# Kernel optimization log

Measured on AMD Instinct MI355X. Metric: run time of the kernel, lower is better.

Reference implementation:

```python
import jax, jax.numpy as jnp
import numpy as np

NUM_NODES = 100000
EMBED_DIM = 128
COMP_DIM = 64
T = 8
NSUB = 50000


def layer_norm(x, g, b, eps=1e-5):
    mu = jnp.mean(x, axis=-1, keepdims=True)
    var = jnp.mean((x - mu) ** 2, axis=-1, keepdims=True)
    return (x - mu) * jax.lax.rsqrt(var + eps) * g + b


def setup_inputs() -> dict:
    key = jax.random.key(0)
    ks = jax.random.split(key, 12)
    D, C = EMBED_DIM, COMP_DIM
    s = lambda n: 1.0 / np.sqrt(n)
    return {
        "x": jax.random.normal(ks[0], (T * NSUB, D), dtype=jnp.float32),
        "indices": jax.random.randint(ks[1], (T, NSUB), 0, NUM_NODES, dtype=jnp.int64),
        "bd": jax.random.normal(ks[2], (NUM_NODES, D), dtype=jnp.float32),
        "ln_d_g": jnp.ones((D,), jnp.float32), "ln_d_b": jnp.zeros((D,), jnp.float32),
        "Wd1": jax.random.normal(ks[3], (D, 2 * D), jnp.float32) * s(D),
        "bd1": jnp.zeros((2 * D,), jnp.float32),
        "Wd2": jax.random.normal(ks[4], (2 * D, C), jnp.float32) * s(2 * D),
        "bd2": jnp.zeros((C,), jnp.float32),
        "ln_u_g": jnp.ones((C,), jnp.float32), "ln_u_b": jnp.zeros((C,), jnp.float32),
        "Wu1": jax.random.normal(ks[5], (C, 2 * C), jnp.float32) * s(C),
        "bu1": jnp.zeros((2 * C,), jnp.float32),
        "Wu2": jax.random.normal(ks[6], (2 * C, D), jnp.float32) * s(2 * C),
        "bu2": jnp.zeros((D,), jnp.float32),
    }


def reference(x, indices, bd, ln_d_g, ln_d_b, Wd1, bd1, Wd2, bd2,
              ln_u_g, ln_u_b, Wu1, bu1, Wu2, bu2):
    # _to_entire: per-timestep scatter-add of subnode feats into full node table
    x3 = x.reshape(T, NSUB, EMBED_DIM)  # [T, Nsub, D]
    scattered = jax.vmap(
        lambda xt, it: jax.ops.segment_sum(xt, it, num_segments=NUM_NODES)
    )(x3, indices)  # [T, num_nodes, D]
    inp = scattered + bd[None]  # ta + bd (use_bd=True)
    h = layer_norm(inp, ln_d_g, ln_d_b)
    # mlp_d: Linear -> GELU -> Dropout(eval=identity) -> Linear
    h = jax.nn.gelu(h @ Wd1 + bd1, approximate=False) @ Wd2 + bd2  # [T, num_nodes, C]
    # _from_entire: gather activated rows per timestep, then LN + mlp_u
    gathered = jax.vmap(lambda ht, it: ht[it])(h, indices)  # [T, Nsub, C]
    g = gathered.reshape(T * NSUB, COMP_DIM)
    u = layer_norm(g, ln_u_g, ln_u_b)
    out = jax.nn.gelu(u @ Wu1 + bu1, approximate=False) @ Wu2 + bu2  # [T*Nsub, D]
    return out
```

## Files before the change

### kernel.cpp

```cpp
#include <hip/hip_runtime.h>
#include <math.h>

#define NN 100000
#define DD 128
#define CC 64
#define TT 8
#define NS 50000
#define G8 8
#define MAXS 391
#define MAXS_B 196
#define T1MAX (G8 * MAXS)
#define T2MAX (G8 * MAXS_B)
#define L2CAP 25000
#define ZINT4 200032

typedef __attribute__((ext_vector_type(4))) float f32x4;
typedef __attribute__((ext_vector_type(8))) short bf16x8;
typedef unsigned short ushort_t;

__device__ __forceinline__ short f2bf(float f) {
    union { float f; unsigned u; } v; v.f = f;
    unsigned r = v.u + 0x7fffu + ((v.u >> 16) & 1u);
    return (short)(r >> 16);
}
__device__ __forceinline__ unsigned pk_bf16(float lo, float hi) {
    unsigned r;
    asm("v_cvt_pk_bf16_f32 %0, %1, %2" : "=v"(r) : "v"(lo), "v"(hi));
    return r;
}
__device__ __forceinline__ float gelu(float x) {
    float t = x + 0.044715f * x * x * x;
    return x / (1.0f + __expf(-1.5957691216f * t));
}

__global__ void prep_all(const float* __restrict__ Wd1, const float* __restrict__ Wd2,
                         const float* __restrict__ Wu1, const float* __restrict__ Wu2,
                         short* __restrict__ pW1, short* __restrict__ pW2,
                         short* __restrict__ pW3, short* __restrict__ pW4,
                         int4* __restrict__ zbase) {
    int b = blockIdx.x;
    if (b >= 36) {
        int i = (b - 36) * 256 + threadIdx.x;
        if (i < ZINT4) zbase[i] = (int4){0, 0, 0, 0};
// ... 57 lines not shown
}

__device__ __forceinline__ void ln_d_pack(
    const float (&v)[32], int kgrp,
    const float* __restrict__ lndg, const float* __restrict__ lndb, bf16x8 (&afr)[4]) {
    float s1 = 0.f;
    #pragma unroll
    for (int j = 0; j < 32; ++j) s1 += v[j];
    s1 += __shfl_xor(s1, 16); s1 += __shfl_xor(s1, 32);
    float mu = s1 * 0.0078125f;
    float s2 = 0.f;
    #pragma unroll
    for (int j = 0; j < 32; ++j) { float d = v[j] - mu; s2 += d * d; }
    s2 += __shfl_xor(s2, 16); s2 += __shfl_xor(s2, 32);
    float rs = rsqrtf(s2 * 0.0078125f + 1e-5f);
    union U8 { bf16x8 v8; unsigned u[4]; };
    const float* gp = lndg + kgrp * 8;
    const float* bbp = lndb + kgrp * 8;
    #pragma unroll
    for (int ks = 0; ks < 4; ++ks) {
        float4 g0 = *(const float4*)(gp + ks * 32);
        float4 g1 = *(const float4*)(gp + ks * 32 + 4);
        float4 c0 = *(const float4*)(bbp + ks * 32);
        float4 c1 = *(const float4*)(bbp + ks * 32 + 4);
        U8 t;
        t.u[0] = pk_bf16((v[ks*8+0]-mu)*rs*g0.x + c0.x, (v[ks*8+1]-mu)*rs*g0.y + c0.y);
        t.u[1] = pk_bf16((v[ks*8+2]-mu)*rs*g0.z + c0.z, (v[ks*8+3]-mu)*rs*g0.w + c0.w);
        t.u[2] = pk_bf16((v[ks*8+4]-mu)*rs*g1.x + c1.x, (v[ks*8+5]-mu)*rs*g1.y + c1.y);
        t.u[3] = pk_bf16((v[ks*8+6]-mu)*rs*g1.z + c1.z, (v[ks*8+7]-mu)*rs*g1.w + c1.w);
        afr[ks] = t.v8;
    }
}

__device__ __forceinline__ void mlp_core(
    const bf16x8 (&afr)[4], short* myb, int arow, int kgrp,
    const short* sW1, const short* sW2, const short* __restrict__ pW3, const short* sW4,
    const float* __restrict__ bd1, const float* __restrict__ bd2,
    const float* __restrict__ lnug, const float* __restrict__ lnub,
    const float* __restrict__ bu1, f32x4 (&acc4)[8]) {
    const int lane = kgrp * 16 + arow;
    f32x4 acc2[4];
    #pragma unroll
    for (int n = 0; n < 4; ++n) acc2[n] = (f32x4){0.f, 0.f, 0.f, 0.f};
    for (int ks2 = 0; ks2 < 8; ++ks2) {
        f32x4 a1v[2];
        a1v[0] = (f32x4){0.f, 0.f, 0.f, 0.f};
        a1v[1] = (f32x4){0.f, 0.f, 0.f, 0.f};
        #pragma unroll
        for (int ks1 = 0; ks1 < 4; ++ks1) {
            #pragma unroll
            for (int p = 0; p < 2; ++p) {
                bf16x8 bf = *(const bf16x8*)(sW1 + (size_t)((((2 * ks2 + p) << 2) | ks1) * 64 + lane) * 8);
                a1v[p] = __builtin_amdgcn_mfma_f32_16x16x32_bf16(afr[ks1], bf, a1v[p], 0, 0, 0);
            }
        }
        #pragma unroll
        for (int p = 0; p < 2; ++p) {
            float bias = bd1[(2 * ks2 + p) * 16 + arow];
            #pragma unroll
            for (int rr = 0; rr < 4; ++rr) {
                float vv = gelu(a1v[p][rr] + bias);
                int row = kgrp * 4 + rr;
                int byte = row * 64 + (((p * 16 + arow) * 2) ^ ((row & 3) << 4));
                myb[byte >> 1] = f2bf(vv);
            }
        }
        bf16x8 af2 = *(const bf16x8*)(myb + ((arow * 64 + ((kgrp * 16) ^ ((arow & 3) << 4))) >> 1));
        #pragma unroll
        for (int n2 = 0; n2 < 4; ++n2) {
            bf16x8 bf = *(const bf16x8*)(sW2 + (size_t)(((n2 << 3) | ks2) * 64 + lane) * 8);
            acc2[n2] = __builtin_amdgcn_mfma_f32_16x16x32_bf16(af2, bf, acc2[n2], 0, 0, 0);
        }
    }
    float hv[4][4];
    #pragma unroll
    for (int n2 = 0; n2 < 4; ++n2)
        #pragma unroll
        for (int rr = 0; rr < 4; ++rr)
            hv[n2][rr] = acc2[n2][rr] + bd2[n2 * 16 + arow];
    #pragma unroll
    for (int rr = 0; rr < 4; ++rr) {
        float sr = hv[0][rr] + hv[1][rr] + hv[2][rr] + hv[3][rr];
        sr += __shfl_xor(sr, 1); sr += __shfl_xor(sr, 2);
        sr += __shfl_xor(sr, 4); sr += __shfl_xor(sr, 8);
        float mu_u = sr * 0.015625f;
        float sq = 0.f;
        #pragma unroll
        for (int n2 = 0; n2 < 4; ++n2) { float d = hv[n2][rr] - mu_u; sq += d * d; }
        sq += __shfl_xor(sq, 1); sq += __shfl_xor(sq, 2);
        sq += __shfl_xor(sq, 4); sq += __shfl_xor(sq, 8);
        float rs_u = rsqrtf(sq * 0.015625f + 1e-5f);
        #pragma unroll
        for (int n2 = 0; n2 < 4; ++n2) {
            int cidx = n2 * 16 + arow;
            float nv = (hv[n2][rr] - mu_u) * rs_u * lnug[cidx] + lnub[cidx];
            int row = kgrp * 4 + rr;
            int byte = row * 128 + ((cidx * 2) ^ ((row & 7) << 4));
            myb[byte >> 1] = f2bf(nv);
        }
    }
    bf16x8 af3[2];
    #pragma unroll
    for (int ks3 = 0; ks3 < 2; ++ks3)
        af3[ks3] = *(const bf16x8*)(myb + ((arow * 128 + ((ks3 * 64 + kgrp * 16) ^ ((arow & 7) << 4))) >> 1));
    #pragma unroll
    for (int n = 0; n < 8; ++n) acc4[n] = (f32x4){0.f, 0.f, 0.f, 0.f};
    #pragma unroll
    for (int half = 0; half < 2; ++half) {
        f32x4 a3[4];
        #pragma unroll
        for (int n = 0; n < 4; ++n) a3[n] = (f32x4){0.f, 0.f, 0.f, 0.f};
        #pragma unroll
        for (int ks3 = 0; ks3 < 2; ++ks3) {
            #pragma unroll
            for (int n3h = 0; n3h < 4; ++n3h) {
                int n3 = half * 4 + n3h;
                bf16x8 bf = *(const bf16x8*)(pW3 + (size_t)(((n3 << 1) | ks3) * 64 + lane) * 8);
                a3[n3h] = __builtin_amdgcn_mfma_f32_16x16x32_bf16(af3[ks3], bf, a3[n3h], 0, 0, 0);
            }
        }
        #pragma unroll
        for (int n3h = 0; n3h < 4; ++n3h) {
            float bias = bu1[(half * 4 + n3h) * 16 + arow];
            #pragma unroll
            for (int rr = 0; rr < 4; ++rr) {
                float vv = gelu(a3[n3h][rr] + bias);
                int row = kgrp * 4 + rr;
                int byte = row * 128 + (((n3h * 16 + arow) * 2) ^ ((row & 7) << 4));
                myb[byte >> 1] = f2bf(vv);
            }
        }
        #pragma unroll
        for (int k4 = 0; k4 < 2; ++k4) {
            bf16x8 afu = *(const bf16x8*)(myb + ((arow * 128 + ((k4 * 64 + kgrp * 16) ^ ((arow & 7) << 4))) >> 1));
            #pragma unroll
            for (int n4 = 0; n4 < 8; ++n4) {
                bf16x8 bf = *(const bf16x8*)(sW4 + (size_t)(((n4 << 2) | (half * 2 + k4)) * 64 + lane) * 8);
                acc4[n4] = __builtin_amdgcn_mfma_f32_16x16x32_bf16(afu, bf, acc4[n4], 0, 0, 0);
            }
        }
    }
}

__global__ __launch_bounds__(512, 2) void fused_kernel(
    const float* __restrict__ x, const float* __restrict__ bd,
    const float* __restrict__ lndg, const float* __restrict__ lndb,
    const short* __restrict__ pW1, const short* __restrict__ pW2,
    const short* __restrict__ pW3, const short* __restrict__ pW4,
    const float* __restrict__ bd1, const float* __restrict__ bd2,
    const float* __restrict__ lnug, const float* __restrict__ lnub,
    const float* __restrict__ bu1, const float* __restrict__ bu2,
    const int2* __restrict__ list1, const int* __restrict__ cnts1,
    const int* __restrict__ list2, const int* __restrict__ cnts2,
    const int* __restrict__ pernode, const ushort_t* __restrict__ bucket,
    float* __restrict__ out) {
    __shared__ short sW1[4096 * 8];
    __shared__ short sW2[2048 * 8];
    __shared__ short sW4[2048 * 8];
    __shared__ short sBuf[8][1024];

    const int tid = threadIdx.x;
    for (int s = tid; s < 4096; s += 512)
        *(bf16x8*)(sW1 + s * 8) = *(const bf16x8*)(pW1 + (size_t)s * 8);
    for (int s = tid; s < 2048; s += 512)
        *(bf16x8*)(sW2 + s * 8) = *(const bf16x8*)(pW2 + (size_t)s * 8);
    for (int s = tid; s < 2048; s += 512)
        *(bf16x8*)(sW4 + s * 8) = *(const bf16x8*)(pW4 + (size_t)s * 8);
    __syncthreads();

    const int wave = tid >> 6, lane = tid & 63;
    short* myb = sBuf[wave];
    float* mf = (float*)myb;
    const int arow = lane & 15;
    const int kgrp = lane >> 4;
    const int q32 = lane >> 5, c32 = lane & 31;

    for (int w = blockIdx.x; w < T1MAX + T2MAX; w += gridDim.x) {
        const bool segA = w < T1MAX;
        int g, row0, nrow;
        if (segA) {
            g = w & 7; row0 = (w >> 3) * 128 + wave * 16; nrow = cnts1[g];
        } else {
            int w2 = w - T1MAX;
            g = w2 & 7; row0 = (w2 >> 3) * 128 + wave * 16; nrow = cnts2[g];
        }
        if (row0 >= nrow) continue;
        const float* x_g = x + (size_t)g * NS * DD;
        float* out_g = out + (size_t)g * NS * DD;
        const int gi = row0 + arow;
        const int gidx = gi < nrow ? gi : nrow - 1;

        int node, c = 1, pos0;
        int4 p8 = (int4){0, 0, 0, 0};
        if (segA) {
            int2 pn = list1[(size_t)g * NS + gidx];
            pos0 = pn.x; node = pn.y;
        } else {
            node = list2[(size_t)g * L2CAP + gidx];
            c = pernode[node * 8 + g];
            p8 = *(const int4*)(bucket + ((size_t)node * 8 + g) * 16);
            pos0 = p8.x & 0xffff;
        }

        float v[32];
        {
            const float* xp = x_g + (size_t)pos0 * DD + kgrp * 8;
            const float* bp = bd + (size_t)node * DD + kgrp * 8;
            #pragma unroll
            for (int ks = 0; ks < 4; ++ks) {
                float4 a0 = *(const float4*)(xp + ks * 32);
                float4 a1 = *(const float4*)(xp + ks * 32 + 4);
                float4 b0 = *(const float4*)(bp + ks * 32);
                float4 b1 = *(const float4*)(bp + ks * 32 + 4);
                v[ks*8+0] = a0.x + b0.x; v[ks*8+1] = a0.y + b0.y;
                v[ks*8+2] = a0.z + b0.z; v[ks*8+3] = a0.w + b0.w;
                v[ks*8+4] = a1.x + b1.x; v[ks*8+5] = a1.y + b1.y;
                v[ks*8+6] = a1.z + b1.z; v[ks*8+7] = a1.w + b1.w;
            }
        }
        if (!segA) {
            const int pr1 = ((unsigned)p8.x) >> 16;
            {
                const float* xq1 = x_g + (size_t)pr1 * DD + kgrp * 8;
                #pragma unroll
                for (int ks = 0; ks < 4; ++ks) {
                    float4 d0 = *(const float4*)(xq1 + ks * 32);
                    float4 d1 = *(const float4*)(xq1 + ks * 32 + 4);
                    v[ks*8+0] += d0.x; v[ks*8+1] += d0.y;
                    v[ks*8+2] += d0.z; v[ks*8+3] += d0.w;
                    v[ks*8+4] += d1.x; v[ks*8+5] += d1.y;
                    v[ks*8+6] += d1.z; v[ks*8+7] += d1.w;
                }
            }
            if (__any(c > 2)) {
                const int pr2 = p8.y & 0xffff, pr3 = ((unsigned)p8.y) >> 16;
                const float* xq2 = x_g + (size_t)((c > 2) ? pr2 : pos0) * DD + kgrp * 8;
                const float* xq3 = x_g + (size_t)((c > 3) ? pr3 : pos0) * DD + kgrp * 8;
                const float m2 = (c > 2) ? 1.f : 0.f;
                const float m3 = (c > 3) ? 1.f : 0.f;
                #pragma unroll
                for (int ks = 0; ks < 4; ++ks) {
                    float4 a0 = *(const float4*)(xq2 + ks * 32);
                    float4 a1 = *(const float4*)(xq2 + ks * 32 + 4);
                    float4 d0 = *(const float4*)(xq3 + ks * 32);
                    float4 d1 = *(const float4*)(xq3 + ks * 32 + 4);
                    v[ks*8+0] = fmaf(m3, d0.x, fmaf(m2, a0.x, v[ks*8+0]));
                    v[ks*8+1] = fmaf(m3, d0.y, fmaf(m2, a0.y, v[ks*8+1]));
                    v[ks*8+2] = fmaf(m3, d0.z, fmaf(m2, a0.z, v[ks*8+2]));
                    v[ks*8+3] = fmaf(m3, d0.w, fmaf(m2, a0.w, v[ks*8+3]));
                    v[ks*8+4] = fmaf(m3, d1.x, fmaf(m2, a1.x, v[ks*8+4]));
                    v[ks*8+5] = fmaf(m3, d1.y, fmaf(m2, a1.y, v[ks*8+5]));
                    v[ks*8+6] = fmaf(m3, d1.z, fmaf(m2, a1.z, v[ks*8+6]));
                    v[ks*8+7] = fmaf(m3, d1.w, fmaf(m2, a1.w, v[ks*8+7]));
                }
            }
            if (__any(c > 4)) {
                const ushort_t* bt = bucket + ((size_t)node * 8 + g) * 16;
                for (int j = 4; j < 16; j += 2) {
                    if (!__any(c > j)) break;
                    const int pa = (j < c) ? bt[j] : pos0;
                    const int pb = (j + 1 < c) ? bt[j + 1] : pos0;
                    const float ma = (j < c) ? 1.f : 0.f;
                    const float mb = (j + 1 < c) ? 1.f : 0.f;
                    const float* xqa = x_g + (size_t)pa * DD + kgrp * 8;
                    const float* xqb = x_g + (size_t)pb * DD + kgrp * 8;
                    #pragma unroll
                    for (int ks = 0; ks < 4; ++ks) {
                        float4 a0 = *(const float4*)(xqa + ks * 32);
                        float4 a1 = *(const float4*)(xqa + ks * 32 + 4);
                        float4 d0 = *(const float4*)(xqb + ks * 32);
                        float4 d1 = *(const float4*)(xqb + ks * 32 + 4);
                        v[ks*8+0] = fmaf(mb, d0.x, fmaf(ma, a0.x, v[ks*8+0]));
                        v[ks*8+1] = fmaf(mb, d0.y, fmaf(ma, a0.y, v[ks*8+1]));
                        v[ks*8+2] = fmaf(mb, d0.z, fmaf(ma, a0.z, v[ks*8+2]));
                        v[ks*8+3] = fmaf(mb, d0.w, fmaf(ma, a0.w, v[ks*8+3]));
                        v[ks*8+4] = fmaf(mb, d1.x, fmaf(ma, a1.x, v[ks*8+4]));
                        v[ks*8+5] = fmaf(mb, d1.y, fmaf(ma, a1.y, v[ks*8+5]));
                        v[ks*8+6] = fmaf(mb, d1.z, fmaf(ma, a1.z, v[ks*8+6]));
                        v[ks*8+7] = fmaf(mb, d1.w, fmaf(ma, a1.w, v[ks*8+7]));
                    }
                }
            }
        }

        bf16x8 afr[4];
        ln_d_pack(v, kgrp, lndg, lndb, afr);
        f32x4 acc4[8];
        mlp_core(afr, myb, arow, kgrp, sW1, sW2, pW3, sW4,
                 bd1, bd2, lnug, lnub, bu1, acc4);

        #pragma unroll
        for (int rr = 0; rr < 4; ++rr) {
            #pragma unroll
            for (int n4 = 0; n4 < 8; ++n4) {
                int col = n4 * 16 + arow;
                int blk = (col >> 2) ^ kgrp;
                mf[kgrp * 128 + blk * 4 + (col & 3)] = acc4[n4][rr] + bu2[col];
            }
            #pragma unroll
            for (int pair = 0; pair < 2; ++pair) {
                int slot = pair * 2 + q32;
                int src = slot * 4 + rr;
                bool valid = (row0 + src) < nrow;
                float4 val = *(const float4*)(mf + slot * 128 + ((c32 ^ slot) * 4));
                if (segA) {
                    int p0v = __shfl(pos0, src);
                    if (valid)
                        *(float4*)(out_g + (size_t)p0v * DD + c32 * 4) = val;
                } else {
                    int c2 = __shfl(c, src);
                    if (!valid) c2 = 0;
                    unsigned u0 = (unsigned)__shfl(p8.x, src);
                    unsigned u1 = (unsigned)__shfl(p8.y, src);
                    unsigned u2 = (unsigned)__shfl(p8.z, src);
                    unsigned u3 = (unsigned)__shfl(p8.w, src);
                    if (c2 > 0) *(float4*)(out_g + (size_t)(u0 & 0xffff) * DD + c32 * 4) = val;
                    if (c2 > 1) *(float4*)(out_g + (size_t)(u0 >> 16) * DD + c32 * 4) = val;
                    if (c2 > 2) *(float4*)(out_g + (size_t)(u1 & 0xffff) * DD + c32 * 4) = val;
                    if (c2 > 3) *(float4*)(out_g + (size_t)(u1 >> 16) * DD + c32 * 4) = val;
                    if (__any(c2 > 4)) {
                        if (c2 > 4) *(float4*)(out_g + (size_t)(u2 & 0xffff) * DD + c32 * 4) = val;
                        if (c2 > 5) *(float4*)(out_g + (size_t)(u2 >> 16) * DD + c32 * 4) = val;
                        if (c2 > 6) *(float4*)(out_g + (size_t)(u3 & 0xffff) * DD + c32 * 4) = val;
                        if (c2 > 7) *(float4*)(out_g + (size_t)(u3 >> 16) * DD + c32 * 4) = val;
                    }
                    if (__any(c2 > 8)) {
                        int nd2 = __shfl(node, src);
                        const ushort_t* bt = bucket + ((size_t)nd2 * 8 + g) * 16;
                        for (int j = 8; j < 16; ++j) {
                            if (!__any(j < c2)) break;
                            if (j < c2)
                                *(float4*)(out_g + (size_t)bt[j] * DD + c32 * 4) = val;
                        }
                    }
                }
            }
        }
    }
}

extern "C" void kernel_launch(void* const* d_in, const int* in_sizes, int n_in,
                              void* d_out, int out_size, void* d_ws, size_t ws_size,
                              hipStream_t stream) {
    const float* x       = (const float*)d_in[0];
    const int*   indices = (const int*)d_in[1];
    const float* bd      = (const float*)d_in[2];
    const float* ln_d_g  = (const float*)d_in[3];
    const float* ln_d_b  = (const float*)d_in[4];
    const float* Wd1     = (const float*)d_in[5];
    const float* bd1     = (const float*)d_in[6];
    const float* Wd2     = (const float*)d_in[7];
    const float* bd2     = (const float*)d_in[8];
    const float* ln_u_g  = (const float*)d_in[9];
    const float* ln_u_b  = (const float*)d_in[10];
    const float* Wu1     = (const float*)d_in[11];
    const float* bu1     = (const float*)d_in[12];
    const float* Wu2     = (const float*)d_in[13];
    const float* bu2     = (const float*)d_in[14];
    float* out = (float*)d_out;

    char* ws = (char*)d_ws;
    size_t o = 0;
    auto alloc_b = [&](size_t bytes) { char* p = ws + o; o = (o + bytes + 255) & ~(size_t)255; return p; };
    int*      pernode = (int*)alloc_b((size_t)NN * 8 * 4);
    int*      cnts1   = (int*)alloc_b(8 * 4);
    int*      cnts2   = (int*)alloc_b(8 * 4);
    int2*     list1   = (int2*)alloc_b((size_t)8 * NS * 8);
    int*      list2   = (int*)alloc_b((size_t)8 * L2CAP * 4);
    ushort_t* bucket  = (ushort_t*)alloc_b((size_t)NN * 8 * 16 * 2);
    short*    pW1     = (short*)alloc_b((size_t)4096 * 16);
// ... 18 lines not shown
```

Measured before the change: 421.2 us.

## Process two 16-row tiles per wave to reuse weight fragments across MFMAs

Each wave now handles two 16-row tiles (A and B) at once. Every B-operand weight fragment loaded from LDS or global memory feeds two MFMAs instead of one, which halves weight-load traffic per row and gives the matrix units more independent work to interleave. The per-segment tile counts (MAXS) are halved to match. This roughly doubles accumulator and activation register use, which may raise register pressure or cause spills under launch_bounds(512,2), and each wave needs a second scratch buffer for tile B.

```diff
diff --git a/kernel.cpp b/kernel.cpp
--- a/kernel.cpp
+++ b/kernel.cpp
@@ -7,8 +7,8 @@
 #define TT 8
 #define NS 50000
 #define G8 8
-#define MAXS 391
-#define MAXS_B 196
+#define MAXS 196
+#define MAXS_B 98
 #define T1MAX (G8 * MAXS)
 #define T2MAX (G8 * MAXS_B)
 #define L2CAP 25000
@@ -132,26 +132,31 @@
     }
 }
 
-__device__ __forceinline__ void mlp_core(
-    const bf16x8 (&afr)[4], short* myb, int arow, int kgrp,
+__device__ __forceinline__ void mlp_core2(
+    const bf16x8 (&afrA)[4], const bf16x8 (&afrB)[4],
+    short* mybA, short* mybB, int arow, int kgrp,
     const short* sW1, const short* sW2, const short* __restrict__ pW3, const short* sW4,
     const float* __restrict__ bd1, const float* __restrict__ bd2,
     const float* __restrict__ lnug, const float* __restrict__ lnub,
-    const float* __restrict__ bu1, f32x4 (&acc4)[8]) {
+    const float* __restrict__ bu1, f32x4 (&acc4A)[8], f32x4 (&acc4B)[8]) {
     const int lane = kgrp * 16 + arow;
-    f32x4 acc2[4];
-    #pragma unroll
-    for (int n = 0; n < 4; ++n) acc2[n] = (f32x4){0.f, 0.f, 0.f, 0.f};
+    f32x4 acc2A[4], acc2B[4];
+    #pragma unroll
+    for (int n = 0; n < 4; ++n) {
+        acc2A[n] = (f32x4){0.f, 0.f, 0.f, 0.f};
+        acc2B[n] = (f32x4){0.f, 0.f, 0.f, 0.f};
+    }
     for (int ks2 = 0; ks2 < 8; ++ks2) {
-        f32x4 a1v[2];
-        a1v[0] = (f32x4){0.f, 0.f, 0.f, 0.f};
-        a1v[1] = (f32x4){0.f, 0.f, 0.f, 0.f};
+        f32x4 a1A[2], a1B[2];
+        a1A[0] = (f32x4){0.f, 0.f, 0.f, 0.f}; a1A[1] = a1A[0];
+        a1B[0] = a1A[0]; a1B[1] = a1A[0];
         #pragma unroll
         for (int ks1 = 0; ks1 < 4; ++ks1) {
             #pragma unroll
             for (int p = 0; p < 2; ++p) {
                 bf16x8 bf = *(const bf16x8*)(sW1 + (size_t)((((2 * ks2 + p) << 2) | ks1) * 64 + lane) * 8);
-                a1v[p] = __builtin_amdgcn_mfma_f32_16x16x32_bf16(afr[ks1], bf, a1v[p], 0, 0, 0);
+                a1A[p] = __builtin_amdgcn_mfma_f32_16x16x32_bf16(afrA[ks1], bf, a1A[p], 0, 0, 0);
+                a1B[p] = __builtin_amdgcn_mfma_f32_16x16x32_bf16(afrB[ks1], bf, a1B[p], 0, 0, 0);
             }
         }
         #pragma unroll
@@ -159,64 +164,90 @@
             float bias = bd1[(2 * ks2 + p) * 16 + arow];
             #pragma unroll
             for (int rr = 0; rr < 4; ++rr) {
-                float vv = gelu(a1v[p][rr] + bias);
                 int row = kgrp * 4 + rr;
-                int byte = row * 64 + (((p * 16 + arow) * 2) ^ ((row & 3) << 4));
-                myb[byte >> 1] = f2bf(vv);
+                int off = (row * 64 + (((p * 16 + arow) * 2) ^ ((row & 3) << 4))) >> 1;
+                mybA[off] = f2bf(gelu(a1A[p][rr] + bias));
+                mybB[off] = f2bf(gelu(a1B[p][rr] + bias));
             }
         }
-        bf16x8 af2 = *(const bf16x8*)(myb + ((arow * 64 + ((kgrp * 16) ^ ((arow & 3) << 4))) >> 1));
+        int roff = (arow * 64 + ((kgrp * 16) ^ ((arow & 3) << 4))) >> 1;
+        bf16x8 af2A = *(const bf16x8*)(mybA + roff);
+        bf16x8 af2B = *(const bf16x8*)(mybB + roff);
         #pragma unroll
         for (int n2 = 0; n2 < 4; ++n2) {
             bf16x8 bf = *(const bf16x8*)(sW2 + (size_t)(((n2 << 3) | ks2) * 64 + lane) * 8);
-            acc2[n2] = __builtin_amdgcn_mfma_f32_16x16x32_bf16(af2, bf, acc2[n2], 0, 0, 0);
-        }
-    }
-    float hv[4][4];
+            acc2A[n2] = __builtin_amdgcn_mfma_f32_16x16x32_bf16(af2A, bf, acc2A[n2], 0, 0, 0);
+            acc2B[n2] = __builtin_amdgcn_mfma_f32_16x16x32_bf16(af2B, bf, acc2B[n2], 0, 0, 0);
+        }
+    }
+    float hvA[4][4], hvB[4][4];
     #pragma unroll
     for (int n2 = 0; n2 < 4; ++n2)
         #pragma unroll
-        for (int rr = 0; rr < 4; ++rr)
-            hv[n2][rr] = acc2[n2][rr] + bd2[n2 * 16 + arow];
+        for (int rr = 0; rr < 4; ++rr) {
+            float b2 = bd2[n2 * 16 + arow];
+            hvA[n2][rr] = acc2A[n2][rr] + b2;
+            hvB[n2][rr] = acc2B[n2][rr] + b2;
+        }
     #pragma unroll
     for (int rr = 0; rr < 4; ++rr) {
-        float sr = hv[0][rr] + hv[1][rr] + hv[2][rr] + hv[3][rr];
-        sr += __shfl_xor(sr, 1); sr += __shfl_xor(sr, 2);
-        sr += __shfl_xor(sr, 4); sr += __shfl_xor(sr, 8);
-        float mu_u = sr * 0.015625f;
-        float sq = 0.f;
-        #pragma unroll
-        for (int n2 = 0; n2 < 4; ++n2) { float d = hv[n2][rr] - mu_u; sq += d * d; }
-        sq += __shfl_xor(sq, 1); sq += __shfl_xor(sq, 2);
-        sq += __shfl_xor(sq, 4); sq += __shfl_xor(sq, 8);
-        float rs_u = rsqrtf(sq * 0.015625f + 1e-5f);
+        float srA = hvA[0][rr] + hvA[1][rr] + hvA[2][rr] + hvA[3][rr];
+        float srB = hvB[0][rr] + hvB[1][rr] + hvB[2][rr] + hvB[3][rr];
+        srA += __shfl_xor(srA, 1); srB += __shfl_xor(srB, 1);
+        srA += __shfl_xor(srA, 2); srB += __shfl_xor(srB, 2);
+        srA += __shfl_xor(srA, 4); srB += __shfl_xor(srB, 4);
+        srA += __shfl_xor(srA, 8); srB += __shfl_xor(srB, 8);
+        float muA = srA * 0.015625f, muB = srB * 0.015625f;
+        float sqA = 0.f, sqB = 0.f;
+        #pragma unroll
+        for (int n2 = 0; n2 < 4; ++n2) {
+            float dA = hvA[n2][rr] - muA; sqA += dA * dA;
+            float dB = hvB[n2][rr] - muB; sqB += dB * dB;
+        }
+        sqA += __shfl_xor(sqA, 1); sqB += __shfl_xor(sqB, 1);
+        sqA += __shfl_xor(sqA, 2); sqB += __shfl_xor(sqB, 2);
+        sqA += __shfl_xor(sqA, 4); sqB += __shfl_xor(sqB, 4);
+        sqA += __shfl_xor(sqA, 8); sqB += __shfl_xor(sqB, 8);
+        float rsA = rsqrtf(sqA * 0.015625f + 1e-5f);
+        float rsB = rsqrtf(sqB * 0.015625f + 1e-5f);
         #pragma unroll
         for (int n2 = 0; n2 < 4; ++n2) {
             int cidx = n2 * 16 + arow;
-            float nv = (hv[n2][rr] - mu_u) * rs_u * lnug[cidx] + lnub[cidx];
+            float gg = lnug[cidx], bb = lnub[cidx];
             int row = kgrp * 4 + rr;
-            int byte = row * 128 + ((cidx * 2) ^ ((row & 7) << 4));
-            myb[byte >> 1] = f2bf(nv);
-        }
-    }
-    bf16x8 af3[2];
-    #pragma unroll
-    for (int ks3 = 0; ks3 < 2; ++ks3)
-        af3[ks3] = *(const bf16x8*)(myb + ((arow * 128 + ((ks3 * 64 + kgrp * 16) ^ ((arow & 7) << 4))) >> 1));
-    #pragma unroll
-    for (int n = 0; n < 8; ++n) acc4[n] = (f32x4){0.f, 0.f, 0.f, 0.f};
+            int off = (row * 128 + ((cidx * 2) ^ ((row & 7) << 4))) >> 1;
+            mybA[off] = f2bf((hvA[n2][rr] - muA) * rsA * gg + bb);
+            mybB[off] = f2bf((hvB[n2][rr] - muB) * rsB * gg + bb);
+        }
+    }
+    bf16x8 af3A[2], af3B[2];
+    #pragma unroll
+    for (int ks3 = 0; ks3 < 2; ++ks3) {
+        int off = (arow * 128 + ((ks3 * 64 + kgrp * 16) ^ ((arow & 7) << 4))) >> 1;
+        af3A[ks3] = *(const bf16x8*)(mybA + off);
+        af3B[ks3] = *(const bf16x8*)(mybB + off);
+    }
+    #pragma unroll
+    for (int n = 0; n < 8; ++n) {
+        acc4A[n] = (f32x4){0.f, 0.f, 0.f, 0.f};
+        acc4B[n] = (f32x4){0.f, 0.f, 0.f, 0.f};
+    }
     #pragma unroll
     for (int half = 0; half < 2; ++half) {
-        f32x4 a3[4];
-        #pragma unroll
-        for (int n = 0; n < 4; ++n) a3[n] = (f32x4){0.f, 0.f, 0.f, 0.f};
+        f32x4 a3A[4], a3B[4];
+        #pragma unroll
+        for (int n = 0; n < 4; ++n) {
+            a3A[n] = (f32x4){0.f, 0.f, 0.f, 0.f};
+            a3B[n] = (f32x4){0.f, 0.f, 0.f, 0.f};
+        }
         #pragma unroll
         for (int ks3 = 0; ks3 < 2; ++ks3) {
             #pragma unroll
             for (int n3h = 0; n3h < 4; ++n3h) {
                 int n3 = half * 4 + n3h;
                 bf16x8 bf = *(const bf16x8*)(pW3 + (size_t)(((n3 << 1) | ks3) * 64 + lane) * 8);
-                a3[n3h] = __builtin_amdgcn_mfma_f32_16x16x32_bf16(af3[ks3], bf, a3[n3h], 0, 0, 0);
+                a3A[n3h] = __builtin_amdgcn_mfma_f32_16x16x32_bf16(af3A[ks3], bf, a3A[n3h], 0, 0, 0);
+                a3B[n3h] = __builtin_amdgcn_mfma_f32_16x16x32_bf16(af3B[ks3], bf, a3B[n3h], 0, 0, 0);
             }
         }
         #pragma unroll
@@ -224,23 +255,162 @@
             float bias = bu1[(half * 4 + n3h) * 16 + arow];
             #pragma unroll
             for (int rr = 0; rr < 4; ++rr) {
-                float vv = gelu(a3[n3h][rr] + bias);
                 int row = kgrp * 4 + rr;
-                int byte = row * 128 + (((n3h * 16 + arow) * 2) ^ ((row & 7) << 4));
-                myb[byte >> 1] = f2bf(vv);
+                int off = (row * 128 + (((n3h * 16 + arow) * 2) ^ ((row & 7) << 4))) >> 1;
+                mybA[off] = f2bf(gelu(a3A[n3h][rr] + bias));
+                mybB[off] = f2bf(gelu(a3B[n3h][rr] + bias));
             }
         }
         #pragma unroll
         for (int k4 = 0; k4 < 2; ++k4) {
-            bf16x8 afu = *(const bf16x8*)(myb + ((arow * 128 + ((k4 * 64 + kgrp * 16) ^ ((arow & 7) << 4))) >> 1));
+            int off = (arow * 128 + ((k4 * 64 + kgrp * 16) ^ ((arow & 7) << 4))) >> 1;
+            bf16x8 afuA = *(const bf16x8*)(mybA + off);
+            bf16x8 afuB = *(const bf16x8*)(mybB + off);
             #pragma unroll
             for (int n4 = 0; n4 < 8; ++n4) {
                 bf16x8 bf = *(const bf16x8*)(sW4 + (size_t)(((n4 << 2) | (half * 2 + k4)) * 64 + lane) * 8);
-                acc4[n4] = __builtin_amdgcn_mfma_f32_16x16x32_bf16(afu, bf, acc4[n4], 0, 0, 0);
+                acc4A[n4] = __builtin_amdgcn_mfma_f32_16x16x32_bf16(afuA, bf, acc4A[n4], 0, 0, 0);
+                acc4B[n4] = __builtin_amdgcn_mfma_f32_16x16x32_bf16(afuB, bf, acc4B[n4], 0, 0, 0);
             }
         }
     }
 }
+
+__device__ __forceinline__ void epilogue_tile(
+    const f32x4 (&acc4)[8], float* mf, int arow, int kgrp, int q32, int c32,
+    int row0s, int nrow, bool segA, int pos0, int c, int4 p8, int node, int g,
+    const float* __restrict__ bu2, const ushort_t* __restrict__ bucket,
+    float* __restrict__ out_g) {
+    #pragma unroll
+    for (int rr = 0; rr < 4; ++rr) {
+        #pragma unroll
+        for (int n4 = 0; n4 < 8; ++n4) {
+            int col = n4 * 16 + arow;
+            int blk = (col >> 2) ^ kgrp;
+            mf[kgrp * 128 + blk * 4 + (col & 3)] = acc4[n4][rr] + bu2[col];
+        }
+        #pragma unroll
+        for (int pair = 0; pair < 2; ++pair) {
+            int slot = pair * 2 + q32;
+            int src = slot * 4 + rr;
+            bool valid = (row0s + src) < nrow;
+            float4 val = *(const float4*)(mf + slot * 128 + ((c32 ^ slot) * 4));
+            if (segA) {
+                int p0v = __shfl(pos0, src);
+                if (valid)
+                    *(float4*)(out_g + (size_t)p0v * DD + c32 * 4) = val;
+            } else {
+                int c2 = __shfl(c, src);
+                if (!valid) c2 = 0;
+                unsigned u0 = (unsigned)__shfl(p8.x, src);
+                unsigned u1 = (unsigned)__shfl(p8.y, src);
+                unsigned u2 = (unsigned)__shfl(p8.z, src);
+                unsigned u3 = (unsigned)__shfl(p8.w, src);
+                if (c2 > 0) *(float4*)(out_g + (size_t)(u0 & 0xffff) * DD + c32 * 4) = val;
+                if (c2 > 1) *(float4*)(out_g + (size_t)(u0 >> 16) * DD + c32 * 4) = val;
+                if (c2 > 2) *(float4*)(out_g + (size_t)(u1 & 0xffff) * DD + c32 * 4) = val;
+                if (c2 > 3) *(float4*)(out_g + (size_t)(u1 >> 16) * DD + c32 * 4) = val;
+                if (__any(c2 > 4)) {
+                    if (c2 > 4) *(float4*)(out_g + (size_t)(u2 & 0xffff) * DD + c32 * 4) = val;
+                    if (c2 > 5) *(float4*)(out_g + (size_t)(u2 >> 16) * DD + c32 * 4) = val;
+                    if (c2 > 6) *(float4*)(out_g + (size_t)(u3 & 0xffff) * DD + c32 * 4) = val;
+                    if (c2 > 7) *(float4*)(out_g + (size_t)(u3 >> 16) * DD + c32 * 4) = val;
+                }
+                if (__any(c2 > 8)) {
+                    int nd2 = __shfl(node, src);
+                    const ushort_t* bt = bucket + ((size_t)nd2 * 8 + g) * 16;
+                    for (int j = 8; j < 16; ++j) {
+                        if (!__any(j < c2)) break;
+                        if (j < c2)
+                            *(float4*)(out_g + (size_t)bt[j] * DD + c32 * 4) = val;
+                    }
+                }
+            }
+        }
+    }
+}
+
+#define GATHER_BASE(vv, posv, nodev)                                            \
+    {                                                                           \
+        const float* xp_ = x_g + (size_t)(posv) * DD + kgrp * 8;                \
+        const float* bp_ = bd + (size_t)(nodev) * DD + kgrp * 8;                \
+        _Pragma("unroll")                                                       \
+        for (int ks = 0; ks < 4; ++ks) {                                        \
+            float4 a0 = *(const float4*)(xp_ + ks * 32);                        \
+            float4 a1 = *(const float4*)(xp_ + ks * 32 + 4);                    \
+            float4 b0 = *(const float4*)(bp_ + ks * 32);                        \
+            float4 b1 = *(const float4*)(bp_ + ks * 32 + 4);                    \
+            vv[ks*8+0] = a0.x + b0.x; vv[ks*8+1] = a0.y + b0.y;                 \
+            vv[ks*8+2] = a0.z + b0.z; vv[ks*8+3] = a0.w + b0.w;                 \
+            vv[ks*8+4] = a1.x + b1.x; vv[ks*8+5] = a1.y + b1.y;                 \
+            vv[ks*8+6] = a1.z + b1.z; vv[ks*8+7] = a1.w + b1.w;                 \
+        }                                                                       \
+    }
+
+#define GATHER_EXTRA(vv, cv, p8v, nodev, posv)                                  \
+    {                                                                           \
+        const int pr1_ = ((unsigned)(p8v).x) >> 16;                             \
+        const float* x1_ = x_g + (size_t)pr1_ * DD + kgrp * 8;                  \
+        _Pragma("unroll")                                                       \
+        for (int ks = 0; ks < 4; ++ks) {                                        \
+            float4 d0 = *(const float4*)(x1_ + ks * 32);                        \
+            float4 d1 = *(const float4*)(x1_ + ks * 32 + 4);                    \
+            vv[ks*8+0] += d0.x; vv[ks*8+1] += d0.y;                             \
+            vv[ks*8+2] += d0.z; vv[ks*8+3] += d0.w;                             \
+            vv[ks*8+4] += d1.x; vv[ks*8+5] += d1.y;                             \
+            vv[ks*8+6] += d1.z; vv[ks*8+7] += d1.w;                             \
+        }                                                                       \
+        if (__any((cv) > 2)) {                                                  \
+            const int pr2_ = (p8v).y & 0xffff;                                  \
+            const int pr3_ = ((unsigned)(p8v).y) >> 16;                         \
+            const float* x2_ = x_g + (size_t)((cv) > 2 ? pr2_ : (posv)) * DD + kgrp * 8; \
+            const float* x3_ = x_g + (size_t)((cv) > 3 ? pr3_ : (posv)) * DD + kgrp * 8; \
+            const float m2_ = (cv) > 2 ? 1.f : 0.f;                             \
+            const float m3_ = (cv) > 3 ? 1.f : 0.f;                             \
+            _Pragma("unroll")                                                   \
+            for (int ks = 0; ks < 4; ++ks) {                                    \
+                float4 a0 = *(const float4*)(x2_ + ks * 32);                    \
+                float4 a1 = *(const float4*)(x2_ + ks * 32 + 4);                \
+                float4 d0 = *(const float4*)(x3_ + ks * 32);                    \
+                float4 d1 = *(const float4*)(x3_ + ks * 32 + 4);                \
+                vv[ks*8+0] = fmaf(m3_, d0.x, fmaf(m2_, a0.x, vv[ks*8+0]));      \
+                vv[ks*8+1] = fmaf(m3_, d0.y, fmaf(m2_, a0.y, vv[ks*8+1]));      \
+                vv[ks*8+2] = fmaf(m3_, d0.z, fmaf(m2_, a0.z, vv[ks*8+2]));      \
+                vv[ks*8+3] = fmaf(m3_, d0.w, fmaf(m2_, a0.w, vv[ks*8+3]));      \
+                vv[ks*8+4] = fmaf(m3_, d1.x, fmaf(m2_, a1.x, vv[ks*8+4]));      \
+                vv[ks*8+5] = fmaf(m3_, d1.y, fmaf(m2_, a1.y, vv[ks*8+5]));      \
+                vv[ks*8+6] = fmaf(m3_, d1.z, fmaf(m2_, a1.z, vv[ks*8+6]));      \
+                vv[ks*8+7] = fmaf(m3_, d1.w, fmaf(m2_, a1.w, vv[ks*8+7]));      \
+            }                                                                   \
+        }                                                                       \
+        if (__any((cv) > 4)) {                                                  \
+            const ushort_t* bt_ = bucket + ((size_t)(nodev) * 8 + g) * 16;      \
+            for (int j = 4; j < 16; j += 2) {                                   \
+                if (!__any((cv) > j)) break;                                    \
+                const int pa_ = (j < (cv)) ? bt_[j] : (posv);                   \
+                const int pb_ = (j + 1 < (cv)) ? bt_[j + 1] : (posv);           \
+                const float ma_ = (j < (cv)) ? 1.f : 0.f;                       \
+                const float mb_ = (j + 1 < (cv)) ? 1.f : 0.f;                   \
+                const float* xa_ = x_g + (size_t)pa_ * DD + kgrp * 8;           \
+                const float* xb_ = x_g + (size_t)pb_ * DD + kgrp * 8;           \
+                _Pragma("unroll")                                               \
+                for (int ks = 0; ks < 4; ++ks) {                                \
+                    float4 a0 = *(const float4*)(xa_ + ks * 32);                \
+                    float4 a1 = *(const float4*)(xa_ + ks * 32 + 4);            \
+                    float4 d0 = *(const float4*)(xb_ + ks * 32);                \
+                    float4 d1 = *(const float4*)(xb_ + ks * 32 + 4);            \
+                    vv[ks*8+0] = fmaf(mb_, d0.x, fmaf(ma_, a0.x, vv[ks*8+0]));  \
+                    vv[ks*8+1] = fmaf(mb_, d0.y, fmaf(ma_, a0.y, vv[ks*8+1]));  \
+                    vv[ks*8+2] = fmaf(mb_, d0.z, fmaf(ma_, a0.z, vv[ks*8+2]));  \
+                    vv[ks*8+3] = fmaf(mb_, d0.w, fmaf(ma_, a0.w, vv[ks*8+3]));  \
+                    vv[ks*8+4] = fmaf(mb_, d1.x, fmaf(ma_, a1.x, vv[ks*8+4]));  \
+                    vv[ks*8+5] = fmaf(mb_, d1.y, fmaf(ma_, a1.y, vv[ks*8+5]));  \
+                    vv[ks*8+6] = fmaf(mb_, d1.z, fmaf(ma_, a1.z, vv[ks*8+6]));  \
+                    vv[ks*8+7] = fmaf(mb_, d1.w, fmaf(ma_, a1.w, vv[ks*8+7]));  \
+                }                                                               \
+            }                                                                   \
+        }                                                                       \
+    }
 
 __global__ __launch_bounds__(512, 2) void fused_kernel(
     const float* __restrict__ x, const float* __restrict__ bd,
@@ -257,7 +427,7 @@
     __shared__ short sW1[4096 * 8];
     __shared__ short sW2[2048 * 8];
     __shared__ short sW4[2048 * 8];
-    __shared__ short sBuf[8][1024];
+    __shared__ short sBuf[8][2048];
 
     const int tid = threadIdx.x;
     for (int s = tid; s < 4096; s += 512)
@@ -269,8 +439,8 @@
     __syncthreads();
 
     const int wave = tid >> 6, lane = tid & 63;
-    short* myb = sBuf[wave];
-    float* mf = (float*)myb;
+    short* mybA = sBuf[wave];
+    short* mybB = sBuf[wave] + 1024;
     const int arow = lane & 15;
     const int kgrp = lane >> 4;
     const int q32 = lane >> 5, c32 = lane & 31;
@@ -279,163 +449,59 @@
         const bool segA = w < T1MAX;
         int g, row0, nrow;
         if (segA) {
-            g = w & 7; row0 = (w >> 3) * 128 + wave * 16; nrow = cnts1[g];
+            g = w & 7; row0 = (w >> 3) * 256 + wave * 32; nrow = cnts1[g];
         } else {
             int w2 = w - T1MAX;
-            g = w2 & 7; row0 = (w2 >> 3) * 128 + wave * 16; nrow = cnts2[g];
+            g = w2 & 7; row0 = (w2 >> 3) * 256 + wave * 32; nrow = cnts2[g];
         }
         if (row0 >= nrow) continue;
         const float* x_g = x + (size_t)g * NS * DD;
         float* out_g = out + (size_t)g * NS * DD;
-        const int gi = row0 + arow;
-        const int gidx = gi < nrow ? gi : nrow - 1;
-
-        int node, c = 1, pos0;
-        int4 p8 = (int4){0, 0, 0, 0};
+        const int giA = row0 + arow;
+        const int giB = row0 + 16 + arow;
+        const int gidxA = giA < nrow ? giA : nrow - 1;
+        const int gidxB = giB < nrow ? giB : nrow - 1;
+
+        int nodeA, cA = 1, posA;
+        int nodeB, cB = 1, posB;
+        int4 p8A = (int4){0, 0, 0, 0};
+        int4 p8B = (int4){0, 0, 0, 0};
         if (segA) {
-            int2 pn = list1[(size_t)g * NS + gidx];
-            pos0 = pn.x; node = pn.y;
+            int2 pa = list1[(size_t)g * NS + gidxA];
+            int2 pb = list1[(size_t)g * NS + gidxB];
+            posA = pa.x; nodeA = pa.y;
+            posB = pb.x; nodeB = pb.y;
         } else {
-            node = list2[(size_t)g * L2CAP + gidx];
-            c = pernode[node * 8 + g];
-            p8 = *(const int4*)(bucket + ((size_t)node * 8 + g) * 16);
-            pos0 = p8.x & 0xffff;
-        }
-
-        float v[32];
-        {
-            const float* xp = x_g + (size_t)pos0 * DD + kgrp * 8;
-            const float* bp = bd + (size_t)node * DD + kgrp * 8;
-            #pragma unroll
-            for (int ks = 0; ks < 4; ++ks) {
-                float4 a0 = *(const float4*)(xp + ks * 32);
-                float4 a1 = *(const float4*)(xp + ks * 32 + 4);
-                float4 b0 = *(const float4*)(bp + ks * 32);
-                float4 b1 = *(const float4*)(bp + ks * 32 + 4);
-                v[ks*8+0] = a0.x + b0.x; v[ks*8+1] = a0.y + b0.y;
-                v[ks*8+2] = a0.z + b0.z; v[ks*8+3] = a0.w + b0.w;
-                v[ks*8+4] = a1.x + b1.x; v[ks*8+5] = a1.y + b1.y;
-                v[ks*8+6] = a1.z + b1.z; v[ks*8+7] = a1.w + b1.w;
-            }
-        }
+            nodeA = list2[(size_t)g * L2CAP + gidxA];
+            nodeB = list2[(size_t)g * L2CAP + gidxB];
+            cA = pernode[nodeA * 8 + g];
+            cB = pernode[nodeB * 8 + g];
+            p8A = *(const int4*)(bucket + ((size_t)nodeA * 8 + g) * 16);
+            p8B = *(const int4*)(bucket + ((size_t)nodeB * 8 + g) * 16);
+            posA = p8A.x & 0xffff;
+            posB = p8B.x & 0xffff;
+        }
+
+        float va[32], vb[32];
+        GATHER_BASE(va, posA, nodeA);
+        GATHER_BASE(vb, posB, nodeB);
         if (!segA) {
-            const int pr1 = ((unsigned)p8.x) >> 16;
-            {
-                const float* xq1 = x_g + (size_t)pr1 * DD + kgrp * 8;
-                #pragma unroll
-                for (int ks = 0; ks < 4; ++ks) {
-                    float4 d0 = *(const float4*)(xq1 + ks * 32);
-                    float4 d1 = *(const float4*)(xq1 + ks * 32 + 4);
-                    v[ks*8+0] += d0.x; v[ks*8+1] += d0.y;
-                    v[ks*8+2] += d0.z; v[ks*8+3] += d0.w;
-                    v[ks*8+4] += d1.x; v[ks*8+5] += d1.y;
-                    v[ks*8+6] += d1.z; v[ks*8+7] += d1.w;
-                }
-            }
-            if (__any(c > 2)) {
-                const int pr2 = p8.y & 0xffff, pr3 = ((unsigned)p8.y) >> 16;
-                const float* xq2 = x_g + (size_t)((c > 2) ? pr2 : pos0) * DD + kgrp * 8;
-                const float* xq3 = x_g + (size_t)((c > 3) ? pr3 : pos0) * DD + kgrp * 8;
-                const float m2 = (c > 2) ? 1.f : 0.f;
-                const float m3 = (c > 3) ? 1.f : 0.f;
-                #pragma unroll
-                for (int ks = 0; ks < 4; ++ks) {
-                    float4 a0 = *(const float4*)(xq2 + ks * 32);
-                    float4 a1 = *(const float4*)(xq2 + ks * 32 + 4);
-                    float4 d0 = *(const float4*)(xq3 + ks * 32);
-                    float4 d1 = *(const float4*)(xq3 + ks * 32 + 4);
-                    v[ks*8+0] = fmaf(m3, d0.x, fmaf(m2, a0.x, v[ks*8+0]));
-                    v[ks*8+1] = fmaf(m3, d0.y, fmaf(m2, a0.y, v[ks*8+1]));
-                    v[ks*8+2] = fmaf(m3, d0.z, fmaf(m2, a0.z, v[ks*8+2]));
-                    v[ks*8+3] = fmaf(m3, d0.w, fmaf(m2, a0.w, v[ks*8+3]));
-                    v[ks*8+4] = fmaf(m3, d1.x, fmaf(m2, a1.x, v[ks*8+4]));
-                    v[ks*8+5] = fmaf(m3, d1.y, fmaf(m2, a1.y, v[ks*8+5]));
-                    v[ks*8+6] = fmaf(m3, d1.z, fmaf(m2, a1.z, v[ks*8+6]));
-                    v[ks*8+7] = fmaf(m3, d1.w, fmaf(m2, a1.w, v[ks*8+7]));
-                }
-            }
-            if (__any(c > 4)) {
-                const ushort_t* bt = bucket + ((size_t)node * 8 + g) * 16;
-                for (int j = 4; j < 16; j += 2) {
-                    if (!__any(c > j)) break;
-                    const int pa = (j < c) ? bt[j] : pos0;
-                    const int pb = (j + 1 < c) ? bt[j + 1] : pos0;
-                    const float ma = (j < c) ? 1.f : 0.f;
-                    const float mb = (j + 1 < c) ? 1.f : 0.f;
-                    const float* xqa = x_g + (size_t)pa * DD + kgrp * 8;
-                    const float* xqb = x_g + (size_t)pb * DD + kgrp * 8;
-                    #pragma unroll
-                    for (int ks = 0; ks < 4; ++ks) {
-                        float4 a0 = *(const float4*)(xqa + ks * 32);
-                        float4 a1 = *(const float4*)(xqa + ks * 32 + 4);
-                        float4 d0 = *(const float4*)(xqb + ks * 32);
-                        float4 d1 = *(const float4*)(xqb + ks * 32 + 4);
-                        v[ks*8+0] = fmaf(mb, d0.x, fmaf(ma, a0.x, v[ks*8+0]));
-                        v[ks*8+1] = fmaf(mb, d0.y, fmaf(ma, a0.y, v[ks*8+1]));
-                        v[ks*8+2] = fmaf(mb, d0.z, fmaf(ma, a0.z, v[ks*8+2]));
-                        v[ks*8+3] = fmaf(mb, d0.w, fmaf(ma, a0.w, v[ks*8+3]));
-                        v[ks*8+4] = fmaf(mb, d1.x, fmaf(ma, a1.x, v[ks*8+4]));
-                        v[ks*8+5] = fmaf(mb, d1.y, fmaf(ma, a1.y, v[ks*8+5]));
-                        v[ks*8+6] = fmaf(mb, d1.z, fmaf(ma, a1.z, v[ks*8+6]));
-                        v[ks*8+7] = fmaf(mb, d1.w, fmaf(ma, a1.w, v[ks*8+7]));
-                    }
-                }
-            }
-        }
-
-        bf16x8 afr[4];
-        ln_d_pack(v, kgrp, lndg, lndb, afr);
-        f32x4 acc4[8];
-        mlp_core(afr, myb, arow, kgrp, sW1, sW2, pW3, sW4,
-                 bd1, bd2, lnug, lnub, bu1, acc4);
-
-        #pragma unroll
-        for (int rr = 0; rr < 4; ++rr) {
-            #pragma unroll
-            for (int n4 = 0; n4 < 8; ++n4) {
-                int col = n4 * 16 + arow;
-                int blk = (col >> 2) ^ kgrp;
-                mf[kgrp * 128 + blk * 4 + (col & 3)] = acc4[n4][rr] + bu2[col];
-            }
-            #pragma unroll
-            for (int pair = 0; pair < 2; ++pair) {
-                int slot = pair * 2 + q32;
-                int src = slot * 4 + rr;
-                bool valid = (row0 + src) < nrow;
-                float4 val = *(const float4*)(mf + slot * 128 + ((c32 ^ slot) * 4));
-                if (segA) {
-                    int p0v = __shfl(pos0, src);
-                    if (valid)
-                        *(float4*)(out_g + (size_t)p0v * DD + c32 * 4) = val;
-                } else {
-                    int c2 = __shfl(c, src);
-                    if (!valid) c2 = 0;
-                    unsigned u0 = (unsigned)__shfl(p8.x, src);
-                    unsigned u1 = (unsigned)__shfl(p8.y, src);
-                    unsigned u2 = (unsigned)__shfl(p8.z, src);
-                    unsigned u3 = (unsigned)__shfl(p8.w, src);
-                    if (c2 > 0) *(float4*)(out_g + (size_t)(u0 & 0xffff) * DD + c32 * 4) = val;
-                    if (c2 > 1) *(float4*)(out_g + (size_t)(u0 >> 16) * DD + c32 * 4) = val;
-                    if (c2 > 2) *(float4*)(out_g + (size_t)(u1 & 0xffff) * DD + c32 * 4) = val;
-                    if (c2 > 3) *(float4*)(out_g + (size_t)(u1 >> 16) * DD + c32 * 4) = val;
-                    if (__any(c2 > 4)) {
-                        if (c2 > 4) *(float4*)(out_g + (size_t)(u2 & 0xffff) * DD + c32 * 4) = val;
-                        if (c2 > 5) *(float4*)(out_g + (size_t)(u2 >> 16) * DD + c32 * 4) = val;
-                        if (c2 > 6) *(float4*)(out_g + (size_t)(u3 & 0xffff) * DD + c32 * 4) = val;
-                        if (c2 > 7) *(float4*)(out_g + (size_t)(u3 >> 16) * DD + c32 * 4) = val;
-                    }
-                    if (__any(c2 > 8)) {
-                        int nd2 = __shfl(node, src);
-                        const ushort_t* bt = bucket + ((size_t)nd2 * 8 + g) * 16;
-                        for (int j = 8; j < 16; ++j) {
-                            if (!__any(j < c2)) break;
-                            if (j < c2)
-                                *(float4*)(out_g + (size_t)bt[j] * DD + c32 * 4) = val;
-                        }
-                    }
-                }
-            }
-        }
+            GATHER_EXTRA(va, cA, p8A, nodeA, posA);
+            GATHER_EXTRA(vb, cB, p8B, nodeB, posB);
+        }
+
+        bf16x8 afrA[4], afrB[4];
+        ln_d_pack(va, kgrp, lndg, lndb, afrA);
+        ln_d_pack(vb, kgrp, lndg, lndb, afrB);
+
+        f32x4 acc4A[8], acc4B[8];
+        mlp_core2(afrA, afrB, mybA, mybB, arow, kgrp, sW1, sW2, pW3, sW4,
+                  bd1, bd2, lnug, lnub, bu1, acc4A, acc4B);
+
+        epilogue_tile(acc4A, (float*)mybA, arow, kgrp, q32, c32, row0, nrow,
+                      segA, posA, cA, p8A, nodeA, g, bu2, bucket, out_g);
+        epilogue_tile(acc4B, (float*)mybB, arow, kgrp, q32, c32, row0 + 16, nrow,
+                      segA, posB, cB, p8B, nodeB, g, bu2, bucket, out_g);
     }
 }
 
```

After: 445.5 us. 1.06x slower.

## Compute full hidden layers at once and stream W2 from global memory

Applied to the files above, without the earlier changes.

The first MLP's hidden layer is now computed in a single pass into 16 accumulators and written whole to a larger per-wave LDS buffer. The second MLP's up-projection is likewise done fully before the down-projection, replacing the interleaved chunked loops. W2 is no longer staged in shared memory and is read from global memory instead. This trades fewer LDS round trips and barriers-in-loop for much higher register pressure (16 accumulators) and a larger LDS footprint per block, which may limit occupancy under launch_bounds(512,2).

```diff
diff --git a/kernel.cpp b/kernel.cpp
--- a/kernel.cpp
+++ b/kernel.cpp
@@ -134,41 +134,43 @@
 
 __device__ __forceinline__ void mlp_core(
     const bf16x8 (&afr)[4], short* myb, int arow, int kgrp,
-    const short* sW1, const short* sW2, const short* __restrict__ pW3, const short* sW4,
+    const short* sW1, const short* __restrict__ pW2,
+    const short* __restrict__ pW3, const short* sW4,
     const float* __restrict__ bd1, const float* __restrict__ bd2,
     const float* __restrict__ lnug, const float* __restrict__ lnub,
     const float* __restrict__ bu1, f32x4 (&acc4)[8]) {
     const int lane = kgrp * 16 + arow;
+    f32x4 accH[16];
+    #pragma unroll
+    for (int n = 0; n < 16; ++n) accH[n] = (f32x4){0.f, 0.f, 0.f, 0.f};
+    #pragma unroll
+    for (int ks1 = 0; ks1 < 4; ++ks1) {
+        #pragma unroll
+        for (int n1 = 0; n1 < 16; ++n1) {
+            bf16x8 bf = *(const bf16x8*)(sW1 + (size_t)(((n1 << 2) | ks1) * 64 + lane) * 8);
+            accH[n1] = __builtin_amdgcn_mfma_f32_16x16x32_bf16(afr[ks1], bf, accH[n1], 0, 0, 0);
+        }
+    }
+    #pragma unroll
+    for (int n1 = 0; n1 < 16; ++n1) {
+        float bias = bd1[n1 * 16 + arow];
+        #pragma unroll
+        for (int rr = 0; rr < 4; ++rr) {
+            int row = kgrp * 4 + rr;
+            int byte = row * 512 + (((n1 * 16 + arow) * 2) ^ ((row & 15) << 4));
+            myb[byte >> 1] = f2bf(gelu(accH[n1][rr] + bias));
+        }
+    }
     f32x4 acc2[4];
     #pragma unroll
     for (int n = 0; n < 4; ++n) acc2[n] = (f32x4){0.f, 0.f, 0.f, 0.f};
+    #pragma unroll
     for (int ks2 = 0; ks2 < 8; ++ks2) {
-        f32x4 a1v[2];
-        a1v[0] = (f32x4){0.f, 0.f, 0.f, 0.f};
-        a1v[1] = (f32x4){0.f, 0.f, 0.f, 0.f};
-        #pragma unroll
-        for (int ks1 = 0; ks1 < 4; ++ks1) {
-            #pragma unroll
-            for (int p = 0; p < 2; ++p) {
-                bf16x8 bf = *(const bf16x8*)(sW1 + (size_t)((((2 * ks2 + p) << 2) | ks1) * 64 + lane) * 8);
-                a1v[p] = __builtin_amdgcn_mfma_f32_16x16x32_bf16(afr[ks1], bf, a1v[p], 0, 0, 0);
-            }
-        }
-        #pragma unroll
-        for (int p = 0; p < 2; ++p) {
-            float bias = bd1[(2 * ks2 + p) * 16 + arow];
-            #pragma unroll
-            for (int rr = 0; rr < 4; ++rr) {
-                float vv = gelu(a1v[p][rr] + bias);
-                int row = kgrp * 4 + rr;
-                int byte = row * 64 + (((p * 16 + arow) * 2) ^ ((row & 3) << 4));
-                myb[byte >> 1] = f2bf(vv);
-            }
-        }
-        bf16x8 af2 = *(const bf16x8*)(myb + ((arow * 64 + ((kgrp * 16) ^ ((arow & 3) << 4))) >> 1));
+        int byte = arow * 512 + ((ks2 * 64 + kgrp * 16) ^ ((arow & 15) << 4));
+        bf16x8 af2 = *(const bf16x8*)(myb + (byte >> 1));
         #pragma unroll
         for (int n2 = 0; n2 < 4; ++n2) {
-            bf16x8 bf = *(const bf16x8*)(sW2 + (size_t)(((n2 << 3) | ks2) * 64 + lane) * 8);
+            bf16x8 bf = *(const bf16x8*)(pW2 + (size_t)(((n2 << 3) | ks2) * 64 + lane) * 8);
             acc2[n2] = __builtin_amdgcn_mfma_f32_16x16x32_bf16(af2, bf, acc2[n2], 0, 0, 0);
         }
     }
@@ -199,45 +201,40 @@
             myb[byte >> 1] = f2bf(nv);
         }
     }
-    bf16x8 af3[2];
-    #pragma unroll
-    for (int ks3 = 0; ks3 < 2; ++ks3)
-        af3[ks3] = *(const bf16x8*)(myb + ((arow * 128 + ((ks3 * 64 + kgrp * 16) ^ ((arow & 7) << 4))) >> 1));
+    f32x4 a3[8];
+    #pragma unroll
+    for (int n = 0; n < 8; ++n) a3[n] = (f32x4){0.f, 0.f, 0.f, 0.f};
+    #pragma unroll
+    for (int ks3 = 0; ks3 < 2; ++ks3) {
+        int byte = arow * 128 + ((ks3 * 64 + kgrp * 16) ^ ((arow & 7) << 4));
+        bf16x8 af3 = *(const bf16x8*)(myb + (byte >> 1));
+        #pragma unroll
+        for (int n3 = 0; n3 < 8; ++n3) {
+            bf16x8 bf = *(const bf16x8*)(pW3 + (size_t)(((n3 << 1) | ks3) * 64 + lane) * 8);
+            a3[n3] = __builtin_amdgcn_mfma_f32_16x16x32_bf16(af3, bf, a3[n3], 0, 0, 0);
+        }
+    }
+    short* g3b = myb + 2048;
+    #pragma unroll
+    for (int n3 = 0; n3 < 8; ++n3) {
+        float bias = bu1[n3 * 16 + arow];
+        #pragma unroll
+        for (int rr = 0; rr < 4; ++rr) {
+            int row = kgrp * 4 + rr;
+            int byte = row * 256 + (((n3 * 16 + arow) * 2) ^ ((row & 15) << 4));
+            g3b[byte >> 1] = f2bf(gelu(a3[n3][rr] + bias));
+        }
+    }
     #pragma unroll
     for (int n = 0; n < 8; ++n) acc4[n] = (f32x4){0.f, 0.f, 0.f, 0.f};
     #pragma unroll
-    for (int half = 0; half < 2; ++half) {
-        f32x4 a3[4];
-        #pragma unroll
-        for (int n = 0; n < 4; ++n) a3[n] = (f32x4){0.f, 0.f, 0.f, 0.f};
-        #pragma unroll
-        for (int ks3 = 0; ks3 < 2; ++ks3) {
-            #pragma unroll
-            for (int n3h = 0; n3h < 4; ++n3h) {
-                int n3 = half * 4 + n3h;
-                bf16x8 bf = *(const bf16x8*)(pW3 + (size_t)(((n3 << 1) | ks3) * 64 + lane) * 8);
-                a3[n3h] = __builtin_amdgcn_mfma_f32_16x16x32_bf16(af3[ks3], bf, a3[n3h], 0, 0, 0);
-            }
-        }
-        #pragma unroll
-        for (int n3h = 0; n3h < 4; ++n3h) {
-            float bias = bu1[(half * 4 + n3h) * 16 + arow];
-            #pragma unroll
-            for (int rr = 0; rr < 4; ++rr) {
-                float vv = gelu(a3[n3h][rr] + bias);
-                int row = kgrp * 4 + rr;
-                int byte = row * 128 + (((n3h * 16 + arow) * 2) ^ ((row & 7) << 4));
-                myb[byte >> 1] = f2bf(vv);
-            }
-        }
-        #pragma unroll
-        for (int k4 = 0; k4 < 2; ++k4) {
-            bf16x8 afu = *(const bf16x8*)(myb + ((arow * 128 + ((k4 * 64 + kgrp * 16) ^ ((arow & 7) << 4))) >> 1));
-            #pragma unroll
-            for (int n4 = 0; n4 < 8; ++n4) {
-                bf16x8 bf = *(const bf16x8*)(sW4 + (size_t)(((n4 << 2) | (half * 2 + k4)) * 64 + lane) * 8);
-                acc4[n4] = __builtin_amdgcn_mfma_f32_16x16x32_bf16(afu, bf, acc4[n4], 0, 0, 0);
-            }
+    for (int k4 = 0; k4 < 4; ++k4) {
+        int byte = arow * 256 + ((k4 * 64 + kgrp * 16) ^ ((arow & 15) << 4));
+        bf16x8 afu = *(const bf16x8*)(g3b + (byte >> 1));
+        #pragma unroll
+        for (int n4 = 0; n4 < 8; ++n4) {
+            bf16x8 bf = *(const bf16x8*)(sW4 + (size_t)(((n4 << 2) | k4) * 64 + lane) * 8);
+            acc4[n4] = __builtin_amdgcn_mfma_f32_16x16x32_bf16(afu, bf, acc4[n4], 0, 0, 0);
         }
     }
 }
@@ -255,15 +252,12 @@
     const int* __restrict__ pernode, const ushort_t* __restrict__ bucket,
     float* __restrict__ out) {
     __shared__ short sW1[4096 * 8];
-    __shared__ short sW2[2048 * 8];
     __shared__ short sW4[2048 * 8];
-    __shared__ short sBuf[8][1024];
+    __shared__ short sBuf[8][4096];
 
     const int tid = threadIdx.x;
     for (int s = tid; s < 4096; s += 512)
         *(bf16x8*)(sW1 + s * 8) = *(const bf16x8*)(pW1 + (size_t)s * 8);
-    for (int s = tid; s < 2048; s += 512)
-        *(bf16x8*)(sW2 + s * 8) = *(const bf16x8*)(pW2 + (size_t)s * 8);
     for (int s = tid; s < 2048; s += 512)
         *(bf16x8*)(sW4 + s * 8) = *(const bf16x8*)(pW4 + (size_t)s * 8);
     __syncthreads();
@@ -386,7 +380,7 @@
         bf16x8 afr[4];
         ln_d_pack(v, kgrp, lndg, lndb, afr);
         f32x4 acc4[8];
-        mlp_core(afr, myb, arow, kgrp, sW1, sW2, pW3, sW4,
+        mlp_core(afr, myb, arow, kgrp, sW1, pW2, pW3, sW4,
                  bd1, bd2, lnug, lnub, bu1, acc4);
 
         #pragma unroll
```

After: 817.8 us. 1.94x slower.
